# Optimization experiments

Measured on AMD Instinct MI355X. Metric: run time of the kernel, lower is better.

Reference implementation:

```python
import jax, jax.numpy as jnp
import numpy as np

N = 50000      # nodes
E = 800000     # edges (avg degree 16)
IN, H, OUT = 256, 128, 64
L = 3          # num SAGEConv layers


def setup_inputs() -> dict:
    key = jax.random.key(0)
    ks = jax.random.split(key, 9)
    x = jax.random.normal(ks[0], (N, IN), dtype=jnp.float32)
    edge_index = jax.random.randint(ks[1], (2, E), 0, N, dtype=jnp.int64)
    s_in, s_h = 1.0 / np.sqrt(IN), 1.0 / np.sqrt(H)
    lin0_w = jax.random.normal(ks[2], (IN, H), dtype=jnp.float32) * s_in
    lin0_b = jnp.zeros((H,), dtype=jnp.float32)
    conv_wl = jax.random.normal(ks[3], (L, H, H), dtype=jnp.float32) * s_h  # applied to aggregated neighbors
    conv_bl = jnp.zeros((L, H), dtype=jnp.float32)
    conv_wr = jax.random.normal(ks[4], (L, H, H), dtype=jnp.float32) * s_h  # applied to root (self) features
    lin1_w = jax.random.normal(ks[5], (H, OUT), dtype=jnp.float32) * s_h
    lin1_b = jnp.zeros((OUT,), dtype=jnp.float32)
    return {"x": x, "edge_index": edge_index, "lin0_w": lin0_w, "lin0_b": lin0_b,
            "conv_wl": conv_wl, "conv_bl": conv_bl, "conv_wr": conv_wr,
            "lin1_w": lin1_w, "lin1_b": lin1_b}


def reference(x, edge_index, lin0_w, lin0_b, conv_wl, conv_bl, conv_wr, lin1_w, lin1_b):
    # Inference mode: dropout(p=0.5, training=False) is identity.
    src, dst = edge_index[0], edge_index[1]  # messages flow src -> dst (PyG source_to_target)
    deg = jax.ops.segment_sum(jnp.ones((E,), x.dtype), dst, num_segments=N)
    deg = jnp.maximum(deg, 1.0)[:, None]  # [N,1] avoid div-by-zero for isolated nodes

    h = jax.nn.relu(x @ lin0_w + lin0_b)  # [N,H]
    for i in range(L):
        # SAGEConv: lin_l(mean_agg(neighbors)) + lin_r(self)
        agg = jax.ops.segment_sum(h[src], dst, num_segments=N) / deg  # [N,H]
        h = jax.nn.relu(agg @ conv_wl[i] + conv_bl[i] + h @ conv_wr[i])
    return h @ lin1_w + lin1_b  # [N,OUT]
```

## Files before the change

### kernel.cpp

```cpp
#include <hip/hip_runtime.h>
#include <hip/hip_bf16.h>

#define N_NODES 50000
#define E_EDGES 800000
#define IN_F 256
#define H_F 128
#define OUT_F 64
#define L_LAYERS 3
#define NB_SCAN 49
#define LIN0_BLOCKS 196
#define COUNT_BLOCKS 3125

typedef __attribute__((ext_vector_type(8))) short bf16x8;
typedef __attribute__((ext_vector_type(4))) float f32x4;

static __device__ __forceinline__ float bf2f(unsigned short u) {
    return __uint_as_float(((unsigned int)u) << 16);
}
static __device__ __forceinline__ unsigned short f2bf(float f) {
    unsigned int b = __float_as_uint(f);
    return (unsigned short)((b + 0x7FFFu + ((b >> 16) & 1u)) >> 16);
}

__global__ __launch_bounds__(1024) void scanA_kernel(const int* __restrict__ cnt,
                                                     int* __restrict__ tmp,
                                                     int* __restrict__ bsum) {
    __shared__ int buf[1024];
    const int tid = threadIdx.x;
    const int i = blockIdx.x * 1024 + tid;
    int v = (i < N_NODES) ? cnt[i] : 0;
    buf[tid] = v;
    __syncthreads();
    for (int off = 1; off < 1024; off <<= 1) {
        int t = (tid >= off) ? buf[tid - off] : 0;
        __syncthreads();
        buf[tid] += t;
        __syncthreads();
    }
    tmp[i] = buf[tid];
    if (tid == 1023) bsum[blockIdx.x] = buf[1023];
}

__global__ void scanB_kernel(int* __restrict__ bsum) {
    int t = threadIdx.x;
    int v = (t < NB_SCAN) ? bsum[t] : 0;
    int incl = v;
    for (int off = 1; off < 64; off <<= 1) {
        int u = __shfl_up(incl, off, 64);
        if (t >= off) incl += u;
    }
    if (t < NB_SCAN) bsum[t] = incl - v;
}

__global__ __launch_bounds__(1024) void scanC_kernel(const int* __restrict__ tmp,
                                                     const int* __restrict__ bsum,
                                                     int* __restrict__ row_ptr) {
    const int i = blockIdx.x * 1024 + threadIdx.x;
    if (i < N_NODES) row_ptr[i + 1] = tmp[i] + bsum[i >> 10];
    if (i == 0) row_ptr[0] = 0;
}

__global__ void place2_kernel(const int* __restrict__ ei, const int* __restrict__ row_ptr,
                              const int* __restrict__ rank, int* __restrict__ esrc) {
    int e = blockIdx.x * blockDim.x + threadIdx.x;
    if (e < E_EDGES) {
        int s = ei[e];
        int d = ei[E_EDGES + e];
        esrc[row_ptr[d] + rank[e]] = s;
    }
}

__global__ void prep_all(const float* __restrict__ lin0_w, const float* __restrict__ conv_wl,
                         const float* __restrict__ conv_wr, const float* __restrict__ lin1_w,
                         unsigned short* __restrict__ BpL0, unsigned short* __restrict__ BpCv,
                         unsigned short* __restrict__ BpL1) {
    int gid = blockIdx.x * 256 + threadIdx.x;
    if (gid < 32768) {
        int idx = gid;
        int j = idx & 7, rest = idx >> 3;
        int c = rest & 127, gg = rest >> 7;
        BpL0[idx] = f2bf(lin0_w[(size_t)(gg * 8 + j) * 128 + c]);
    } else if (gid < 32768 + 3 * 32768) {
        int t = gid - 32768;
        int l = t >> 15, idx = t & 32767;
        int j = idx & 7, rest = idx >> 3;
        int c = rest & 127, gg = rest >> 7;
        int k = gg * 8 + j;
        const float* wl = conv_wl + (size_t)l * 16384;
        const float* wr = conv_wr + (size_t)l * 16384;
        float v = (k < 128) ? wl[(size_t)k * 128 + c] : wr[(size_t)(k - 128) * 128 + c];
        BpCv[t] = f2bf(v);
    } else if (gid < 32768 + 3 * 32768 + 8192) {
        int idx = gid - (32768 + 3 * 32768);
        int j = idx & 7, rest = idx >> 3;
        int c = rest & 63, gg = rest >> 6;
        BpL1[idx] = f2bf(lin1_w[(size_t)(gg * 8 + j) * 64 + c]);
    }
}

__global__ __launch_bounds__(256, 8) void agg_kernel(
        const unsigned short* __restrict__ hb, const int* __restrict__ row_ptr,
        const int* __restrict__ esrc, unsigned short* __restrict__ Gb) {
    const int wid = (blockIdx.x * 256 + threadIdx.x) >> 6;
    const int lane = threadIdx.x & 63;
    const int p = lane >> 4;
    const int q = lane & 15;
    const int s0 = row_ptr[wid];
    const int s1 = row_ptr[wid + 1];
    float a[8] = {};
    int j = s0;
    for (; j + 8 <= s1; j += 8) {
        int ea = esrc[j + p];
        int eb = esrc[j + p + 4];
        bf16x8 va = *(const bf16x8*)(hb + ((size_t)ea << 7) + (q << 3));
        bf16x8 vb = *(const bf16x8*)(hb + ((size_t)eb << 7) + (q << 3));
#pragma unroll
        for (int t = 0; t < 8; ++t)
            a[t] += bf2f((unsigned short)va[t]) + bf2f((unsigned short)vb[t]);
    }
    if (j + p < s1) {
        bf16x8 v = *(const bf16x8*)(hb + ((size_t)esrc[j + p] << 7) + (q << 3));
#pragma unroll
        for (int t = 0; t < 8; ++t) a[t] += bf2f((unsigned short)v[t]);
    }
    if (j + p + 4 < s1) {
        bf16x8 v = *(const bf16x8*)(hb + ((size_t)esrc[j + p + 4] << 7) + (q << 3));
#pragma unroll
        for (int t = 0; t < 8; ++t) a[t] += bf2f((unsigned short)v[t]);
    }
#pragma unroll
    for (int t = 0; t < 8; ++t) {
        a[t] += __shfl_xor(a[t], 16, 64);
        a[t] += __shfl_xor(a[t], 32, 64);
    }
    if (p == 0) {
        float dinv = 1.0f / (float)max(s1 - s0, 1);
        bf16x8 o;
#pragma unroll
        for (int t = 0; t < 8; ++t) o[t] = (short)f2bf(a[t] * dinv);
        *(bf16x8*)(Gb + ((size_t)wid << 7) + (q << 3)) = o;
    }
}


__global__ __launch_bounds__(256, 2) void lin0_count(
        const float* __restrict__ x, const unsigned short* __restrict__ Bp,
        const float* __restrict__ bias, unsigned short* __restrict__ hb,
        const int* __restrict__ ei, int* __restrict__ cnt, int* __restrict__ rank) {
    if (blockIdx.x >= LIN0_BLOCKS) {
        int e = (blockIdx.x - LIN0_BLOCKS) * 256 + threadIdx.x;
        if (e < E_EDGES) {
            int d = ei[E_EDGES + e];
            rank[e] = atomicAdd(&cnt[d], 1);
        }
        return;
    }
    const int tid = threadIdx.x;
    const int wave = tid >> 6, lane = tid & 63;
    const int g = lane >> 4, r = lane & 15;
    const int row_base = blockIdx.x * 256 + wave * 64;
    f32x4 acc[4][8] = {};
    for (int kb = 0; kb < 8; ++kb) {
        bf16x8 afr[4];
#pragma unroll
        for (int rt = 0; rt < 4; ++rt) {
            int row = min(row_base + rt * 16 + r, N_NODES - 1);
            const float* ap = x + (size_t)row * IN_F + kb * 32 + g * 8;
            float4 v0 = *(const float4*)ap;
            float4 v1 = *(const float4*)(ap + 4);
            afr[rt][0] = (short)f2bf(v0.x); afr[rt][1] = (short)f2bf(v0.y);
            afr[rt][2] = (short)f2bf(v0.z); afr[rt][3] = (short)f2bf(v0.w);
            afr[rt][4] = (short)f2bf(v1.x); afr[rt][5] = (short)f2bf(v1.y);
            afr[rt][6] = (short)f2bf(v1.z); afr[rt][7] = (short)f2bf(v1.w);
        }
#pragma unroll
        for (int ct = 0; ct < 8; ++ct) {
            bf16x8 bfr = *(const bf16x8*)(Bp + ((size_t)((kb * 4 + g) * H_F) + ct * 16 + r) * 8);
#pragma unroll
            for (int rt = 0; rt < 4; ++rt)
                acc[rt][ct] = __builtin_amdgcn_mfma_f32_16x16x32_bf16(afr[rt], bfr, acc[rt][ct], 0, 0, 0);
        }
    }
#pragma unroll
    for (int ct = 0; ct < 8; ++ct) {
        int col = ct * 16 + r;
        float bv = bias[col];
#pragma unroll
        for (int rt = 0; rt < 4; ++rt)
#pragma unroll
            for (int i = 0; i < 4; ++i) {
                int row = row_base + rt * 16 + g * 4 + i;
                if (row < N_NODES)
                    hb[(size_t)row * H_F + col] = f2bf(fmaxf(acc[rt][ct][i] + bv, 0.f));
            }
    }
}

__global__ __launch_bounds__(256, 2) void conv_mfma(
        const unsigned short* __restrict__ Gb, const unsigned short* __restrict__ hb,
        const unsigned short* __restrict__ Bp, const float* __restrict__ bias,
        unsigned short* __restrict__ hbout) {
    const int tid = threadIdx.x;
    const int wave = tid >> 6, lane = tid & 63;
    const int g = lane >> 4, r = lane & 15;
    const int row_base = blockIdx.x * 256 + wave * 64;
    f32x4 acc[4][8] = {};
    for (int kb = 0; kb < 8; ++kb) {
        const unsigned short* Aptr = (kb < 4) ? Gb : hb;
        const int ko = (kb & 3) * 32 + g * 8;
        bf16x8 afr[4];
#pragma unroll
        for (int rt = 0; rt < 4; ++rt) {
            int row = min(row_base + rt * 16 + r, N_NODES - 1);
            afr[rt] = *(const bf16x8*)(Aptr + (size_t)row * H_F + ko);
        }
#pragma unroll
        for (int ct = 0; ct < 8; ++ct) {
            bf16x8 bfr = *(const bf16x8*)(Bp + ((size_t)((kb * 4 + g) * H_F) + ct * 16 + r) * 8);
#pragma unroll
            for (int rt = 0; rt < 4; ++rt)
                acc[rt][ct] = __builtin_amdgcn_mfma_f32_16x16x32_bf16(afr[rt], bfr, acc[rt][ct], 0, 0, 0);
        }
    }
#pragma unroll
    for (int ct = 0; ct < 8; ++ct) {
        int col = ct * 16 + r;
        float bv = bias[col];
#pragma unroll
        for (int rt = 0; rt < 4; ++rt)
#pragma unroll
            for (int i = 0; i < 4; ++i) {
                int row = row_base + rt * 16 + g * 4 + i;
                if (row < N_NODES)
                    hbout[(size_t)row * H_F + col] = f2bf(fmaxf(acc[rt][ct][i] + bv, 0.f));
            }
    }
}

__global__ __launch_bounds__(256, 2) void lin1_mfma(
        const unsigned short* __restrict__ hb, const unsigned short* __restrict__ Bp,
        const float* __restrict__ bias, float* __restrict__ out) {
    const int tid = threadIdx.x;
    const int wave = tid >> 6, lane = tid & 63;
    const int g = lane >> 4, r = lane & 15;
    const int row_base = blockIdx.x * 256 + wave * 64;
    f32x4 acc[4][4] = {};
    for (int kb = 0; kb < 4; ++kb) {
        const int ko = kb * 32 + g * 8;
        bf16x8 afr[4];
#pragma unroll
        for (int rt = 0; rt < 4; ++rt) {
            int row = min(row_base + rt * 16 + r, N_NODES - 1);
            afr[rt] = *(const bf16x8*)(hb + (size_t)row * H_F + ko);
        }
#pragma unroll
        for (int ct = 0; ct < 4; ++ct) {
            bf16x8 bfr = *(const bf16x8*)(Bp + ((size_t)((kb * 4 + g) * OUT_F) + ct * 16 + r) * 8);
#pragma unroll
            for (int rt = 0; rt < 4; ++rt)
                acc[rt][ct] = __builtin_amdgcn_mfma_f32_16x16x32_bf16(afr[rt], bfr, acc[rt][ct], 0, 0, 0);
        }
    }
#pragma unroll
    for (int ct = 0; ct < 4; ++ct) {
        int col = ct * 16 + r;
        float bv = bias[col];
#pragma unroll
        for (int rt = 0; rt < 4; ++rt)
#pragma unroll
            for (int i = 0; i < 4; ++i) {
                int row = row_base + rt * 16 + g * 4 + i;
                if (row < N_NODES)
                    out[(size_t)row * OUT_F + col] = acc[rt][ct][i] + bv;
            }
    }
}

extern "C" void kernel_launch(void* const* d_in, const int* in_sizes, int n_in,
                              void* d_out, int out_size, void* d_ws, size_t ws_size,
                              hipStream_t stream) {
    const float* x       = (const float*)d_in[0];
    const int*   ei      = (const int*)d_in[1];
    const float* lin0_w  = (const float*)d_in[2];
    const float* lin0_b  = (const float*)d_in[3];
    const float* conv_wl = (const float*)d_in[4];
    const float* conv_bl = (const float*)d_in[5];
    const float* conv_wr = (const float*)d_in[6];
    const float* lin1_w  = (const float*)d_in[7];
    const float* lin1_b  = (const float*)d_in[8];
    float* out = (float*)d_out;

    const size_t NPAD = 50176;
    char* ws = (char*)d_ws;
    size_t off = 0;
    auto alloc = [&](size_t bytes) {
        void* p = ws + off;
        off = (off + bytes + 255) & ~(size_t)255;
        return p;
    };
    int* cnt     = (int*)alloc((size_t)N_NODES * 4);
    int* row_ptr = (int*)alloc((size_t)(N_NODES + 1) * 4);
    int* esrc    = (int*)alloc((size_t)E_EDGES * 4);
    int* rank    = (int*)alloc((size_t)E_EDGES * 4);
    int* tmp     = (int*)alloc((size_t)NB_SCAN * 1024 * 4);
    int* bsum    = (int*)alloc(64 * 4);
    unsigned short* hb0  = (unsigned short*)alloc(NPAD * H_F * 2);
    unsigned short* hb1  = (unsigned short*)alloc(NPAD * H_F * 2);
    unsigned short* Gb   = (unsigned short*)alloc(NPAD * H_F * 2);
    unsigned short* BpL0 = (unsigned short*)alloc((size_t)IN_F * H_F * 2);
    unsigned short* BpCv = (unsigned short*)alloc((size_t)L_LAYERS * 256 * H_F * 2);
    unsigned short* BpL1 = (unsigned short*)alloc((size_t)H_F * OUT_F * 2);

    hipMemsetAsync(cnt, 0, (size_t)N_NODES * 4, stream);
    prep_all<<<544, 256, 0, stream>>>(lin0_w, conv_wl, conv_wr, lin1_w, BpL0, BpCv, BpL1);

    lin0_count<<<LIN0_BLOCKS + COUNT_BLOCKS, 256, 0, stream>>>(
        x, BpL0, lin0_b, hb0, ei, cnt, rank);

    scanA_kernel<<<NB_SCAN, 1024, 0, stream>>>(cnt, tmp, bsum);
    scanB_kernel<<<1, 64, 0, stream>>>(bsum);
    scanC_kernel<<<NB_SCAN, 1024, 0, stream>>>(tmp, bsum, row_ptr);
    place2_kernel<<<COUNT_BLOCKS, 256, 0, stream>>>(ei, row_ptr, rank, esrc);

    const int gemm_grid = (int)(NPAD / 256);

    unsigned short* h = hb0;
    unsigned short* nh = hb1;
    for (int l = 0; l < L_LAYERS; ++l) {
        agg_kernel<<<N_NODES / 4, 256, 0, stream>>>(h, row_ptr, esrc, Gb);
        conv_mfma<<<gemm_grid, 256, 0, stream>>>(Gb, h, BpCv + (size_t)l * 256 * H_F,
                                                 conv_bl + (size_t)l * H_F, nh);
        unsigned short* t = h; h = nh; nh = t;
    }

    lin1_mfma<<<gemm_grid, 256, 0, stream>>>(h, BpL1, lin1_b, out);
}
```

Before: 366.3 us.

## Fuse neighbor aggregation into conv GEMM via LDS and shrink GEMM tiles

Merges the per-layer aggregation kernel into the conv GEMM. Each block now gathers and averages neighbor features for 64 nodes into a swizzled shared-memory tile, then runs the MFMA GEMM from that tile. This removes the Gb intermediate round trip through global memory and one launch per layer. GEMM tiles shrink from 256 to 64 rows per block so there are more blocks and higher occupancy, at the cost of less B-fragment reuse per block. The degree counters are padded to 64 bytes each to reduce atomic contention, which means a 16x larger memset.

Result: no change. 360.3 us (-1.6%).

```diff
diff --git a/kernel.cpp b/kernel.cpp
--- a/kernel.cpp
+++ b/kernel.cpp
@@ -8,8 +8,9 @@
 #define OUT_F 64
 #define L_LAYERS 3
 #define NB_SCAN 49
-#define LIN0_BLOCKS 196
+#define LIN0_BLOCKS 784
 #define COUNT_BLOCKS 3125
+#define NPAD 50176
 
 typedef __attribute__((ext_vector_type(8))) short bf16x8;
 typedef __attribute__((ext_vector_type(4))) float f32x4;
@@ -28,7 +29,7 @@
     __shared__ int buf[1024];
     const int tid = threadIdx.x;
     const int i = blockIdx.x * 1024 + tid;
-    int v = (i < N_NODES) ? cnt[i] : 0;
+    int v = (i < N_NODES) ? cnt[(size_t)i << 4] : 0;
     buf[tid] = v;
     __syncthreads();
     for (int off = 1; off < 1024; off <<= 1) {
@@ -98,52 +99,7 @@
     }
 }
 
-__global__ __launch_bounds__(256, 8) void agg_kernel(
-        const unsigned short* __restrict__ hb, const int* __restrict__ row_ptr,
-        const int* __restrict__ esrc, unsigned short* __restrict__ Gb) {
-    const int wid = (blockIdx.x * 256 + threadIdx.x) >> 6;
-    const int lane = threadIdx.x & 63;
-    const int p = lane >> 4;
-    const int q = lane & 15;
-    const int s0 = row_ptr[wid];
-    const int s1 = row_ptr[wid + 1];
-    float a[8] = {};
-    int j = s0;
-    for (; j + 8 <= s1; j += 8) {
-        int ea = esrc[j + p];
-        int eb = esrc[j + p + 4];
-        bf16x8 va = *(const bf16x8*)(hb + ((size_t)ea << 7) + (q << 3));
-        bf16x8 vb = *(const bf16x8*)(hb + ((size_t)eb << 7) + (q << 3));
-#pragma unroll
-        for (int t = 0; t < 8; ++t)
-            a[t] += bf2f((unsigned short)va[t]) + bf2f((unsigned short)vb[t]);
-    }
-    if (j + p < s1) {
-        bf16x8 v = *(const bf16x8*)(hb + ((size_t)esrc[j + p] << 7) + (q << 3));
-#pragma unroll
-        for (int t = 0; t < 8; ++t) a[t] += bf2f((unsigned short)v[t]);
-    }
-    if (j + p + 4 < s1) {
-        bf16x8 v = *(const bf16x8*)(hb + ((size_t)esrc[j + p + 4] << 7) + (q << 3));
-#pragma unroll
-        for (int t = 0; t < 8; ++t) a[t] += bf2f((unsigned short)v[t]);
-    }
-#pragma unroll
-    for (int t = 0; t < 8; ++t) {
-        a[t] += __shfl_xor(a[t], 16, 64);
-        a[t] += __shfl_xor(a[t], 32, 64);
-    }
-    if (p == 0) {
-        float dinv = 1.0f / (float)max(s1 - s0, 1);
-        bf16x8 o;
-#pragma unroll
-        for (int t = 0; t < 8; ++t) o[t] = (short)f2bf(a[t] * dinv);
-        *(bf16x8*)(Gb + ((size_t)wid << 7) + (q << 3)) = o;
-    }
-}
-
-
-__global__ __launch_bounds__(256, 2) void lin0_count(
+__global__ __launch_bounds__(256, 4) void lin0_count(
         const float* __restrict__ x, const unsigned short* __restrict__ Bp,
         const float* __restrict__ bias, unsigned short* __restrict__ hb,
         const int* __restrict__ ei, int* __restrict__ cnt, int* __restrict__ rank) {
@@ -151,34 +107,29 @@
         int e = (blockIdx.x - LIN0_BLOCKS) * 256 + threadIdx.x;
         if (e < E_EDGES) {
             int d = ei[E_EDGES + e];
-            rank[e] = atomicAdd(&cnt[d], 1);
+            rank[e] = atomicAdd(&cnt[(size_t)d << 4], 1);
         }
         return;
     }
     const int tid = threadIdx.x;
     const int wave = tid >> 6, lane = tid & 63;
     const int g = lane >> 4, r = lane & 15;
-    const int row_base = blockIdx.x * 256 + wave * 64;
-    f32x4 acc[4][8] = {};
+    const int row_base = blockIdx.x * 64 + wave * 16;
+    f32x4 acc[8] = {};
     for (int kb = 0; kb < 8; ++kb) {
-        bf16x8 afr[4];
-#pragma unroll
-        for (int rt = 0; rt < 4; ++rt) {
-            int row = min(row_base + rt * 16 + r, N_NODES - 1);
-            const float* ap = x + (size_t)row * IN_F + kb * 32 + g * 8;
-            float4 v0 = *(const float4*)ap;
-            float4 v1 = *(const float4*)(ap + 4);
-            afr[rt][0] = (short)f2bf(v0.x); afr[rt][1] = (short)f2bf(v0.y);
-            afr[rt][2] = (short)f2bf(v0.z); afr[rt][3] = (short)f2bf(v0.w);
-            afr[rt][4] = (short)f2bf(v1.x); afr[rt][5] = (short)f2bf(v1.y);
-            afr[rt][6] = (short)f2bf(v1.z); afr[rt][7] = (short)f2bf(v1.w);
-        }
+        int row = min(row_base + r, N_NODES - 1);
+        const float* ap = x + (size_t)row * IN_F + kb * 32 + g * 8;
+        float4 v0 = *(const float4*)ap;
+        float4 v1 = *(const float4*)(ap + 4);
+        bf16x8 afr;
+        afr[0] = (short)f2bf(v0.x); afr[1] = (short)f2bf(v0.y);
+        afr[2] = (short)f2bf(v0.z); afr[3] = (short)f2bf(v0.w);
+        afr[4] = (short)f2bf(v1.x); afr[5] = (short)f2bf(v1.y);
+        afr[6] = (short)f2bf(v1.z); afr[7] = (short)f2bf(v1.w);
 #pragma unroll
         for (int ct = 0; ct < 8; ++ct) {
             bf16x8 bfr = *(const bf16x8*)(Bp + ((size_t)((kb * 4 + g) * H_F) + ct * 16 + r) * 8);
-#pragma unroll
-            for (int rt = 0; rt < 4; ++rt)
-                acc[rt][ct] = __builtin_amdgcn_mfma_f32_16x16x32_bf16(afr[rt], bfr, acc[rt][ct], 0, 0, 0);
+            acc[ct] = __builtin_amdgcn_mfma_f32_16x16x32_bf16(afr, bfr, acc[ct], 0, 0, 0);
         }
     }
 #pragma unroll
@@ -186,40 +137,85 @@
         int col = ct * 16 + r;
         float bv = bias[col];
 #pragma unroll
-        for (int rt = 0; rt < 4; ++rt)
-#pragma unroll
-            for (int i = 0; i < 4; ++i) {
-                int row = row_base + rt * 16 + g * 4 + i;
-                if (row < N_NODES)
-                    hb[(size_t)row * H_F + col] = f2bf(fmaxf(acc[rt][ct][i] + bv, 0.f));
-            }
-    }
-}
-
-__global__ __launch_bounds__(256, 2) void conv_mfma(
-        const unsigned short* __restrict__ Gb, const unsigned short* __restrict__ hb,
-        const unsigned short* __restrict__ Bp, const float* __restrict__ bias,
-        unsigned short* __restrict__ hbout) {
+        for (int i = 0; i < 4; ++i) {
+            int row = row_base + g * 4 + i;
+            if (row < N_NODES)
+                hb[(size_t)row * H_F + col] = f2bf(fmaxf(acc[ct][i] + bv, 0.f));
+        }
+    }
+}
+
+__global__ __launch_bounds__(256, 4) void conv_fused(
+        const unsigned short* __restrict__ hb, const int* __restrict__ row_ptr,
+        const int* __restrict__ esrc, const unsigned short* __restrict__ Bp,
+        const float* __restrict__ bias, unsigned short* __restrict__ hbout) {
+    __shared__ unsigned short sAgg[64 * 128];
     const int tid = threadIdx.x;
     const int wave = tid >> 6, lane = tid & 63;
+    const int row0 = blockIdx.x * 64;
+
+    {
+        const int p = lane >> 4;
+        const int q = lane & 15;
+        for (int i = 0; i < 16; ++i) {
+            const int ln = wave * 16 + i;
+            const int node = row0 + ln;
+            int s0 = 0, s1 = 0;
+            if (node < N_NODES) { s0 = row_ptr[node]; s1 = row_ptr[node + 1]; }
+            float a[8] = {};
+            int j = s0;
+            for (; j + 8 <= s1; j += 8) {
+                int ea = esrc[j + p];
+                int eb = esrc[j + p + 4];
+                bf16x8 va = *(const bf16x8*)(hb + ((size_t)ea << 7) + (q << 3));
+                bf16x8 vb = *(const bf16x8*)(hb + ((size_t)eb << 7) + (q << 3));
+#pragma unroll
+                for (int t = 0; t < 8; ++t)
+                    a[t] += bf2f((unsigned short)va[t]) + bf2f((unsigned short)vb[t]);
+            }
+            if (j + p < s1) {
+                bf16x8 v = *(const bf16x8*)(hb + ((size_t)esrc[j + p] << 7) + (q << 3));
+#pragma unroll
+                for (int t = 0; t < 8; ++t) a[t] += bf2f((unsigned short)v[t]);
+            }
+            if (j + p + 4 < s1) {
+                bf16x8 v = *(const bf16x8*)(hb + ((size_t)esrc[j + p + 4] << 7) + (q << 3));
+#pragma unroll
+                for (int t = 0; t < 8; ++t) a[t] += bf2f((unsigned short)v[t]);
+            }
+#pragma unroll
+            for (int t = 0; t < 8; ++t) {
+                a[t] += __shfl_xor(a[t], 16, 64);
+                a[t] += __shfl_xor(a[t], 32, 64);
+            }
+            if (p == 0) {
+                float dinv = 1.0f / (float)max(s1 - s0, 1);
+                bf16x8 o;
+#pragma unroll
+                for (int t = 0; t < 8; ++t) o[t] = (short)f2bf(a[t] * dinv);
+                int c16 = q ^ (ln & 7);
+                *(bf16x8*)(sAgg + ln * 128 + (c16 << 3)) = o;
+            }
+        }
+    }
+    __syncthreads();
+
     const int g = lane >> 4, r = lane & 15;
-    const int row_base = blockIdx.x * 256 + wave * 64;
-    f32x4 acc[4][8] = {};
+    const int row_base = row0 + wave * 16;
+    f32x4 acc[8] = {};
     for (int kb = 0; kb < 8; ++kb) {
-        const unsigned short* Aptr = (kb < 4) ? Gb : hb;
-        const int ko = (kb & 3) * 32 + g * 8;
-        bf16x8 afr[4];
-#pragma unroll
-        for (int rt = 0; rt < 4; ++rt) {
-            int row = min(row_base + rt * 16 + r, N_NODES - 1);
-            afr[rt] = *(const bf16x8*)(Aptr + (size_t)row * H_F + ko);
+        bf16x8 afr;
+        if (kb < 4) {
+            int c16 = (kb * 4 + g) ^ (r & 7);
+            afr = *(const bf16x8*)(sAgg + (wave * 16 + r) * 128 + (c16 << 3));
+        } else {
+            int row = min(row_base + r, N_NODES - 1);
+            afr = *(const bf16x8*)(hb + (size_t)row * H_F + (kb & 3) * 32 + g * 8);
         }
 #pragma unroll
         for (int ct = 0; ct < 8; ++ct) {
             bf16x8 bfr = *(const bf16x8*)(Bp + ((size_t)((kb * 4 + g) * H_F) + ct * 16 + r) * 8);
-#pragma unroll
-            for (int rt = 0; rt < 4; ++rt)
-                acc[rt][ct] = __builtin_amdgcn_mfma_f32_16x16x32_bf16(afr[rt], bfr, acc[rt][ct], 0, 0, 0);
+            acc[ct] = __builtin_amdgcn_mfma_f32_16x16x32_bf16(afr, bfr, acc[ct], 0, 0, 0);
         }
     }
 #pragma unroll
@@ -227,38 +223,29 @@
         int col = ct * 16 + r;
         float bv = bias[col];
 #pragma unroll
-        for (int rt = 0; rt < 4; ++rt)
-#pragma unroll
-            for (int i = 0; i < 4; ++i) {
-                int row = row_base + rt * 16 + g * 4 + i;
-                if (row < N_NODES)
-                    hbout[(size_t)row * H_F + col] = f2bf(fmaxf(acc[rt][ct][i] + bv, 0.f));
-            }
-    }
-}
-
-__global__ __launch_bounds__(256, 2) void lin1_mfma(
+        for (int i = 0; i < 4; ++i) {
+            int row = row_base + g * 4 + i;
+            if (row < N_NODES)
+                hbout[(size_t)row * H_F + col] = f2bf(fmaxf(acc[ct][i] + bv, 0.f));
+        }
+    }
+}
+
+__global__ __launch_bounds__(256, 4) void lin1_mfma(
         const unsigned short* __restrict__ hb, const unsigned short* __restrict__ Bp,
         const float* __restrict__ bias, float* __restrict__ out) {
     const int tid = threadIdx.x;
     const int wave = tid >> 6, lane = tid & 63;
     const int g = lane >> 4, r = lane & 15;
-    const int row_base = blockIdx.x * 256 + wave * 64;
-    f32x4 acc[4][4] = {};
+    const int row_base = blockIdx.x * 64 + wave * 16;
+    f32x4 acc[4] = {};
     for (int kb = 0; kb < 4; ++kb) {
-        const int ko = kb * 32 + g * 8;
-        bf16x8 afr[4];
-#pragma unroll
-        for (int rt = 0; rt < 4; ++rt) {
-            int row = min(row_base + rt * 16 + r, N_NODES - 1);
-            afr[rt] = *(const bf16x8*)(hb + (size_t)row * H_F + ko);
-        }
+        int row = min(row_base + r, N_NODES - 1);
+        bf16x8 afr = *(const bf16x8*)(hb + (size_t)row * H_F + kb * 32 + g * 8);
 #pragma unroll
         for (int ct = 0; ct < 4; ++ct) {
             bf16x8 bfr = *(const bf16x8*)(Bp + ((size_t)((kb * 4 + g) * OUT_F) + ct * 16 + r) * 8);
-#pragma unroll
-            for (int rt = 0; rt < 4; ++rt)
-                acc[rt][ct] = __builtin_amdgcn_mfma_f32_16x16x32_bf16(afr[rt], bfr, acc[rt][ct], 0, 0, 0);
+            acc[ct] = __builtin_amdgcn_mfma_f32_16x16x32_bf16(afr, bfr, acc[ct], 0, 0, 0);
         }
     }
 #pragma unroll
@@ -266,13 +253,11 @@
         int col = ct * 16 + r;
         float bv = bias[col];
 #pragma unroll
-        for (int rt = 0; rt < 4; ++rt)
-#pragma unroll
-            for (int i = 0; i < 4; ++i) {
-                int row = row_base + rt * 16 + g * 4 + i;
-                if (row < N_NODES)
-                    out[(size_t)row * OUT_F + col] = acc[rt][ct][i] + bv;
-            }
+        for (int i = 0; i < 4; ++i) {
+            int row = row_base + g * 4 + i;
+            if (row < N_NODES)
+                out[(size_t)row * OUT_F + col] = acc[ct][i] + bv;
+        }
     }
 }
 
@@ -290,7 +275,6 @@
     const float* lin1_b  = (const float*)d_in[8];
     float* out = (float*)d_out;
 
-    const size_t NPAD = 50176;
     char* ws = (char*)d_ws;
     size_t off = 0;
     auto alloc = [&](size_t bytes) {
@@ -298,20 +282,19 @@
         off = (off + bytes + 255) & ~(size_t)255;
         return p;
     };
-    int* cnt     = (int*)alloc((size_t)N_NODES * 4);
+    int* cnt     = (int*)alloc((size_t)N_NODES * 16 * 4);
     int* row_ptr = (int*)alloc((size_t)(N_NODES + 1) * 4);
     int* esrc    = (int*)alloc((size_t)E_EDGES * 4);
     int* rank    = (int*)alloc((size_t)E_EDGES * 4);
     int* tmp     = (int*)alloc((size_t)NB_SCAN * 1024 * 4);
     int* bsum    = (int*)alloc(64 * 4);
-    unsigned short* hb0  = (unsigned short*)alloc(NPAD * H_F * 2);
-    unsigned short* hb1  = (unsigned short*)alloc(NPAD * H_F * 2);
-    unsigned short* Gb   = (unsigned short*)alloc(NPAD * H_F * 2);
+    unsigned short* hb0  = (unsigned short*)alloc((size_t)NPAD * H_F * 2);
+    unsigned short* hb1  = (unsigned short*)alloc((size_t)NPAD * H_F * 2);
     unsigned short* BpL0 = (unsigned short*)alloc((size_t)IN_F * H_F * 2);
     unsigned short* BpCv = (unsigned short*)alloc((size_t)L_LAYERS * 256 * H_F * 2);
     unsigned short* BpL1 = (unsigned short*)alloc((size_t)H_F * OUT_F * 2);
 
-    hipMemsetAsync(cnt, 0, (size_t)N_NODES * 4, stream);
+    hipMemsetAsync(cnt, 0, (size_t)N_NODES * 16 * 4, stream);
     prep_all<<<544, 256, 0, stream>>>(lin0_w, conv_wl, conv_wr, lin1_w, BpL0, BpCv, BpL1);
 
     lin0_count<<<LIN0_BLOCKS + COUNT_BLOCKS, 256, 0, stream>>>(
@@ -322,16 +305,14 @@
     scanC_kernel<<<NB_SCAN, 1024, 0, stream>>>(tmp, bsum, row_ptr);
     place2_kernel<<<COUNT_BLOCKS, 256, 0, stream>>>(ei, row_ptr, rank, esrc);
 
-    const int gemm_grid = (int)(NPAD / 256);
-
     unsigned short* h = hb0;
     unsigned short* nh = hb1;
     for (int l = 0; l < L_LAYERS; ++l) {
-        agg_kernel<<<N_NODES / 4, 256, 0, stream>>>(h, row_ptr, esrc, Gb);
-        conv_mfma<<<gemm_grid, 256, 0, stream>>>(Gb, h, BpCv + (size_t)l * 256 * H_F,
-                                                 conv_bl + (size_t)l * H_F, nh);
+        conv_fused<<<NPAD / 64, 256, 0, stream>>>(h, row_ptr, esrc,
+                                                  BpCv + (size_t)l * 256 * H_F,
+                                                  conv_bl + (size_t)l * H_F, nh);
         unsigned short* t = h; h = nh; nh = t;
     }
 
-    lin1_mfma<<<gemm_grid, 256, 0, stream>>>(h, BpL1, lin1_b, out);
-}
+    lin1_mfma<<<NPAD / 64, 256, 0, stream>>>(h, BpL1, lin1_b, out);
+}
```
